# Kernel optimization log

Measured on AMD Instinct MI355X. Metric: run time of the kernel, lower is better.

## Reference

```python
import jax, jax.numpy as jnp
import numpy as np


def setup_inputs() -> dict:
    key = jax.random.key(0)
    kA, kB = jax.random.split(key)
    B, H, W, C = 1, 80, 80, 256  # NHWC backbone features; B must be 1 for the TF broadcast in the divide to be valid
    feature_A = jax.random.normal(kA, (B, H, W, C), dtype=jnp.float32)
    feature_B = jax.random.normal(kB, (B, H, W, C), dtype=jnp.float32)
    return {"feature_A": feature_A, "feature_B": feature_B}


def reference(feature_A, feature_B):
    # corr[b,i,j,k,l] = mean_c A[b,i,j,c] * B[b,k,l,c]
    # Expressed as a batched matmul instead of materializing the (H,W,H,W,C) intermediate.
    C = feature_A.shape[-1]
    corr = jnp.einsum('bijc,bklc->bijkl', feature_A, feature_B) / C  # [B,H,W,H,W]
    # penalty[b,i,j] = sqrt(sum_{k,l} corr^2)
    penalty = jnp.sqrt(jnp.sum(corr * corr, axis=(-1, -2)))  # [B,H,W]
    # Faithful to tf.math.divide: trailing-dim broadcasting of [B,H,W] against [B,H,W,H,W]
    # (valid because B == 1; penalty aligns to the (j,k,l) trailing axes exactly as in TF).
    return corr / penalty
```

## Files before the change

kernel.cpp:

```cpp
#include <hip/hip_runtime.h>

typedef __attribute__((ext_vector_type(8))) short bf16x8;
typedef __attribute__((ext_vector_type(4))) float f32x4;

#define M_TOT 6400
#define C_TOT 256
#define BM 128
#define BN 128
#define BK 32
#define NTILE 50
#define GK_CHUNKS 20
#define GK_STEPS  10

#define VMCNT0 asm volatile("s_waitcnt vmcnt(0)" ::: "memory")
#define VMCNT4 asm volatile("s_waitcnt vmcnt(4)" ::: "memory")
#define SBAR   __builtin_amdgcn_s_barrier()

__device__ __forceinline__ short f2bf(float f) {
    unsigned u = __float_as_uint(f);
    u = (u + 0x7fffu + ((u >> 16) & 1u)) >> 16;
    return (short)u;
}
__device__ __forceinline__ float bf2f(short s) {
    return __uint_as_float(((unsigned)(unsigned short)s) << 16);
}

__device__ __forceinline__ void gload16(const short* g, short* l) {
    __builtin_amdgcn_global_load_lds(
        (const __attribute__((address_space(1))) void*)g,
        (__attribute__((address_space(3))) void*)l, 16, 0, 0);
}


__global__ __launch_bounds__(256) void convert_a(const float* __restrict__ A,
                                                 short* __restrict__ Ab)
{
    const int n8 = M_TOT * C_TOT / 8;
    for (int i = blockIdx.x * blockDim.x + threadIdx.x; i < n8;
         i += gridDim.x * blockDim.x) {
        const float4 v0 = reinterpret_cast<const float4*>(A + (size_t)i * 8)[0];
        const float4 v1 = reinterpret_cast<const float4*>(A + (size_t)i * 8)[1];
        bf16x8 w;
        w[0]=f2bf(v0.x); w[1]=f2bf(v0.y); w[2]=f2bf(v0.z); w[3]=f2bf(v0.w);
        w[4]=f2bf(v1.x); w[5]=f2bf(v1.y); w[6]=f2bf(v1.z); w[7]=f2bf(v1.w);
        *reinterpret_cast<bf16x8*>(Ab + (size_t)i * 8) = w;
    }
}

__global__ __launch_bounds__(256) void convert_ab(const float* __restrict__ A,
                                                  const float* __restrict__ Bm,
                                                  short* __restrict__ Ab,
                                                  short* __restrict__ Bb)
{
    const int n8 = M_TOT * C_TOT / 8;
    for (int i = blockIdx.x * blockDim.x + threadIdx.x; i < 2 * n8;
         i += gridDim.x * blockDim.x) {
        const float* s = (i < n8) ? (A + (size_t)i * 8) : (Bm + (size_t)(i - n8) * 8);
        short* d       = (i < n8) ? (Ab + (size_t)i * 8) : (Bb + (size_t)(i - n8) * 8);
        const float4 v0 = reinterpret_cast<const float4*>(s)[0];
        const float4 v1 = reinterpret_cast<const float4*>(s)[1];
        bf16x8 w;
        w[0]=f2bf(v0.x); w[1]=f2bf(v0.y); w[2]=f2bf(v0.z); w[3]=f2bf(v0.w);
        w[4]=f2bf(v1.x); w[5]=f2bf(v1.y); w[6]=f2bf(v1.z); w[7]=f2bf(v1.w);
        *reinterpret_cast<bf16x8*>(d) = w;
    }
}

__global__ __launch_bounds__(256) void trans_b(const float* __restrict__ Bm,
                                               short* __restrict__ Bb,
                                               short* __restrict__ Bt)
{
    __shared__ __align__(16) short Lb[64][72];
    const int t  = threadIdx.x;
    const int n0 = blockIdx.x * 64;
    const int c0 = blockIdx.y * 64;
    const int r  = t >> 2;
    const int cb = (t & 3) * 16;

    const float4* src = reinterpret_cast<const float4*>(
        Bm + (size_t)(n0 + r) * C_TOT + c0 + cb);
    const float4 v0 = src[0], v1 = src[1], v2 = src[2], v3 = src[3];
    bf16x8 w0, w1;
    w0[0]=f2bf(v0.x); w0[1]=f2bf(v0.y); w0[2]=f2bf(v0.z); w0[3]=f2bf(v0.w);
    w0[4]=f2bf(v1.x); w0[5]=f2bf(v1.y); w0[6]=f2bf(v1.z); w0[7]=f2bf(v1.w);
    w1[0]=f2bf(v2.x); w1[1]=f2bf(v2.y); w1[2]=f2bf(v2.z); w1[3]=f2bf(v2.w);
    w1[4]=f2bf(v3.x); w1[5]=f2bf(v3.y); w1[6]=f2bf(v3.z); w1[7]=f2bf(v3.w);
    *reinterpret_cast<bf16x8*>(&Lb[r][cb])     = w0;
    *reinterpret_cast<bf16x8*>(&Lb[r][cb + 8]) = w1;
    short* brow = Bb + (size_t)(n0 + r) * C_TOT + c0 + cb;
    *reinterpret_cast<bf16x8*>(brow)     = w0;
    *reinterpret_cast<bf16x8*>(brow + 8) = w1;
    __syncthreads();

    #pragma unroll
    for (int p = 0; p < 2; ++p) {
        const int q = t + p * 256;
        const int c = q >> 3;
        const int h = q & 7;
        bf16x8 w;
        #pragma unroll
        for (int j = 0; j < 8; ++j) w[j] = Lb[h * 8 + j][c];
        *reinterpret_cast<bf16x8*>(&Bt[(size_t)(c0 + c) * M_TOT + n0 + h * 8]) = w;
    }
}


__device__ __forceinline__ void stage_tiles_g(const short* __restrict__ A,
                                              const short* __restrict__ B,
                                              int m0, int n0, int k0,
                                              int lda, int ldb,
                                              short* As, short* Bs,
                                              int wave, int lane)
{
    #pragma unroll
    for (int t = 0; t < 2; ++t) {
        const int c  = (wave * 2 + t) * 64 + lane;
        const int r  = c >> 2;
        const int g  = c & 3;
        const int sg = g ^ ((r >> 1) & 3);
        gload16(A + (size_t)(m0 + r) * lda + k0 + sg * 8, As + (wave * 2 + t) * 512);
        gload16(B + (size_t)(n0 + r) * ldb + k0 + sg * 8, Bs + (wave * 2 + t) * 512);
    }
}

template<int KSTEPS>
__device__ __forceinline__ void gemm_tile_g(const short* __restrict__ A,
                                            const short* __restrict__ B,
                                            int m0, int n0, int kbase,
                                            int lda, int ldb, int tid,
                                            short (*Sm)[2][4096],
                                            f32x4 acc[4][4])
{
    const int lane = tid & 63;
    const int wave = tid >> 6;
    const int rl   = lane & 15;
    const int g_rd = lane >> 4;
    const int wr   = wave >> 1;
    const int wc   = wave & 1;

    stage_tiles_g(A, B, m0, n0, kbase, lda, ldb, &Sm[0][0][0], &Sm[0][1][0], wave, lane);
    if (KSTEPS > 1)
        stage_tiles_g(A, B, m0, n0, kbase + BK, lda, ldb,
                      &Sm[1][0][0], &Sm[1][1][0], wave, lane);
    if (KSTEPS > 1) { VMCNT4; } else { VMCNT0; }
    SBAR;

    #pragma unroll
    for (int kt = 0; kt < KSTEPS; ++kt) {
        const int cur = kt % 3;
        if (kt + 2 < KSTEPS)
            stage_tiles_g(A, B, m0, n0, kbase + (kt + 2) * BK, lda, ldb,
                          &Sm[(kt + 2) % 3][0][0], &Sm[(kt + 2) % 3][1][0], wave, lane);

        bf16x8 af[4], bfr[4];
        #pragma unroll
        for (int mi = 0; mi < 4; ++mi) {
            const int r  = wr * 64 + mi * 16 + rl;
            const int sg = g_rd ^ ((r >> 1) & 3);
            af[mi] = *reinterpret_cast<const bf16x8*>(&Sm[cur][0][r * BK + sg * 8]);
        }
        #pragma unroll
        for (int ni = 0; ni < 4; ++ni) {
            const int r  = wc * 64 + ni * 16 + rl;
            const int sg = g_rd ^ ((r >> 1) & 3);
            bfr[ni] = *reinterpret_cast<const bf16x8*>(&Sm[cur][1][r * BK + sg * 8]);
        }
        #pragma unroll
        for (int mi = 0; mi < 4; ++mi)
            #pragma unroll
            for (int ni = 0; ni < 4; ++ni)
                acc[mi][ni] = __builtin_amdgcn_mfma_f32_16x16x32_bf16(
                    af[mi], bfr[ni], acc[mi][ni], 0, 0, 0);

        if (kt + 1 < KSTEPS) {
            if (kt + 2 < KSTEPS) { VMCNT4; } else { VMCNT0; }
            SBAR;
        }
    }
}


__global__ __launch_bounds__(256) void gemm_G(const short* __restrict__ Bt,
                                              float* __restrict__ Gp)
{
    __shared__ __align__(16) short Sm[3][2][4096];
    const int tid = threadIdx.x;
    const int m0 = blockIdx.y * BM, n0 = blockIdx.x * BN;
    const int z  = blockIdx.z;
    f32x4 acc[4][4] = {};
    gemm_tile_g<GK_STEPS>(Bt, Bt, m0, n0, z * (M_TOT / GK_CHUNKS),
                          M_TOT, M_TOT, tid, Sm, acc);

    float* dst = Gp + (size_t)z * (C_TOT * C_TOT);
    const int lane = tid & 63, rl = lane & 15;
    const int wave = tid >> 6, wr = wave >> 1, wc = wave & 1;
    #pragma unroll
    for (int mi = 0; mi < 4; ++mi)
        #pragma unroll
        for (int i = 0; i < 4; ++i) {
            const int m = m0 + wr * 64 + mi * 16 + (lane >> 4) * 4 + i;
            #pragma unroll
            for (int ni = 0; ni < 4; ++ni)
                dst[m * C_TOT + n0 + wc * 64 + ni * 16 + rl] = acc[mi][ni][i];
        }
}

__global__ __launch_bounds__(256) void g_reduce(const float* __restrict__ Gp,
                                                short* __restrict__ Gb)
{
    const int i4 = blockIdx.x * 256 + threadIdx.x;
    float4 s = make_float4(0.f, 0.f, 0.f, 0.f);
    for (int z = 0; z < GK_CHUNKS; ++z) {
        const float4 v = reinterpret_cast<const float4*>(
            Gp + (size_t)z * (C_TOT * C_TOT))[i4];
        s.x += v.x; s.y += v.y; s.z += v.z; s.w += v.w;
    }
    short4 o;
    o.x = f2bf(s.x); o.y = f2bf(s.y); o.z = f2bf(s.z); o.w = f2bf(s.w);
    reinterpret_cast<short4*>(Gb)[i4] = o;
}

__global__ __launch_bounds__(256) void penalty_G(const short* __restrict__ Ab,
                                                 const short* __restrict__ Gb,
                                                 float* __restrict__ P)
{
    __shared__ __align__(16) short Sm[3][2][4096];
    __shared__ float q_lds[BM];
    const int tid = threadIdx.x;
    const int m0 = blockIdx.x * BM;
    const int lane = tid & 63, rl = lane & 15;
    const int wave = tid >> 6, wr = wave >> 1, wc = wave & 1;

    if (tid < BM) q_lds[tid] = 0.0f;
    __syncthreads();

    #pragma unroll
    for (int nt = 0; nt < 2; ++nt) {
        f32x4 acc[4][4] = {};
        gemm_tile_g<8>(Ab, Gb, m0, nt * BN, 0, C_TOT, C_TOT, tid, Sm, acc);
        const int n0 = nt * BN;
        #pragma unroll
        for (int mi = 0; mi < 4; ++mi)
            #pragma unroll
            for (int i = 0; i < 4; ++i) {
                const int m = m0 + wr * 64 + mi * 16 + (lane >> 4) * 4 + i;
                float s = 0.0f;
                #pragma unroll
                for (int ni = 0; ni < 4; ++ni) {
                    const int cp = n0 + wc * 64 + ni * 16 + rl;
                    s += acc[mi][ni][i] * bf2f(Ab[(size_t)m * C_TOT + cp]);
                }
                s += __shfl_xor(s, 1);
                s += __shfl_xor(s, 2);
                s += __shfl_xor(s, 4);
                s += __shfl_xor(s, 8);
                if (rl == 0) atomicAdd(&q_lds[m - m0], s);
            }
        __syncthreads();
    }
    if (tid < BM) P[m0 + tid] = q_lds[tid];
}


__global__ __launch_bounds__(256) void gemm_out(const short* __restrict__ Ab,
                                                const short* __restrict__ Bb,
                                                const float* __restrict__ P,
                                                float* __restrict__ out)
{
    __shared__ __align__(16) short Sm[3][2][4096];
    const int tid = threadIdx.x;
    const int lane = tid & 63, rl = lane & 15;
    const int wave = tid >> 6, wr = wave >> 1, wc = wave & 1;

    const int nwg = NTILE * NTILE, q = nwg >> 3, r = nwg & 7;
    const int orig = blockIdx.x;
    const int xcd = orig & 7, idx = orig >> 3;
    const int wg = (xcd < r ? xcd * (q + 1) : r * (q + 1) + (xcd - r) * q) + idx;
    const int m0 = (wg / NTILE) * BM;
    const int n0 = (wg % NTILE) * BN;

    float rs[4];
    #pragma unroll
    for (int ni = 0; ni < 4; ++ni)
        rs[ni] = rsqrtf(P[n0 + wc * 64 + ni * 16 + rl]);

    f32x4 acc[4][4] = {};
    gemm_tile_g<8>(Ab, Bb, m0, n0, 0, C_TOT, C_TOT, tid, Sm, acc);

    SBAR;

    float* Es = reinterpret_cast<float*>(Sm) + wave * 1088;
    #pragma unroll
    for (int mi = 0; mi < 4; ++mi) {
        #pragma unroll
        for (int ni = 0; ni < 4; ++ni)
            #pragma unroll
            for (int i = 0; i < 4; ++i)
                Es[((lane >> 4) * 4 + i) * 68 + ni * 16 + rl] = acc[mi][ni][i] * rs[ni];
        #pragma unroll
        for (int it = 0; it < 4; ++it) {
            const int f   = it * 64 + lane;
            const int row = f >> 4;
            const int c4  = f & 15;
            const float4 v = *reinterpret_cast<const float4*>(&Es[row * 68 + c4 * 4]);
            const int m = m0 + wr * 64 + mi * 16 + row;
            *reinterpret_cast<float4*>(&out[(size_t)m * M_TOT + n0 + wc * 64 + c4 * 4]) = v;
        }
    }
}


__global__ __launch_bounds__(256) void gemm_penalty(const short* __restrict__ Ab,
                                                    const short* __restrict__ Bb,
                                                    float* __restrict__ P)
{
    __shared__ __align__(16) short Sm[3][2][4096];
    const int tid = threadIdx.x;
    const int m0 = blockIdx.y * BM, n0 = blockIdx.x * BN;
    f32x4 acc[4][4] = {};
    gemm_tile_g<8>(Ab, Bb, m0, n0, 0, C_TOT, C_TOT, tid, Sm, acc);

    const int lane = tid & 63, rl = lane & 15;
    const int wave = tid >> 6, wr = wave >> 1;
    #pragma unroll
    for (int mi = 0; mi < 4; ++mi) {
        #pragma unroll
        for (int i = 0; i < 4; ++i) {
            const int m = m0 + wr * 64 + mi * 16 + (lane >> 4) * 4 + i;
            float s = 0.0f;
            #pragma unroll
            for (int ni = 0; ni < 4; ++ni) {
                const float v = acc[mi][ni][i];
                s += v * v;
            }
            s += __shfl_xor(s, 1);
            s += __shfl_xor(s, 2);
            s += __shfl_xor(s, 4);
            s += __shfl_xor(s, 8);
            if (rl == 0) atomicAdd(&P[m], s);
        }
    }
}

__global__ __launch_bounds__(256) void gemm_out_plain(const short* __restrict__ Ab,
                                                      const short* __restrict__ Bb,
                                                      const float* __restrict__ P,
                                                      float* __restrict__ out)
{
    __shared__ __align__(16) short Sm[3][2][4096];
    const int tid = threadIdx.x;
    const int lane = tid & 63, rl = lane & 15;
    const int wave = tid >> 6, wr = wave >> 1, wc = wave & 1;
    const int m0 = blockIdx.y * BM, n0 = blockIdx.x * BN;

    float rs[4];
    #pragma unroll
    for (int ni = 0; ni < 4; ++ni)
        rs[ni] = rsqrtf(P[n0 + wc * 64 + ni * 16 + rl]);

    f32x4 acc[4][4] = {};
    gemm_tile_g<8>(Ab, Bb, m0, n0, 0, C_TOT, C_TOT, tid, Sm, acc);

    SBAR;

    float* Es = reinterpret_cast<float*>(Sm) + wave * 1088;
    #pragma unroll
    for (int mi = 0; mi < 4; ++mi) {
        #pragma unroll
        for (int ni = 0; ni < 4; ++ni)
            #pragma unroll
            for (int i = 0; i < 4; ++i)
                Es[((lane >> 4) * 4 + i) * 68 + ni * 16 + rl] = acc[mi][ni][i] * rs[ni];
        #pragma unroll
        for (int it = 0; it < 4; ++it) {
            const int f   = it * 64 + lane;
            const int row = f >> 4;
            const int c4  = f & 15;
            const float4 v = *reinterpret_cast<const float4*>(&Es[row * 68 + c4 * 4]);
            const int m = m0 + wr * 64 + mi * 16 + row;
            *reinterpret_cast<float4*>(&out[(size_t)m * M_TOT + n0 + wc * 64 + c4 * 4]) = v;
        }
    }
}


__global__ __launch_bounds__(256) void corr_gemm(const float* __restrict__ A,
                                                 const float* __restrict__ Bm,
                                                 float* __restrict__ out,
                                                 float* __restrict__ penalty)
{
    __shared__ short As[BM * BK];
    __shared__ short Bs[BN * BK];

    const int tid  = threadIdx.x;
    const int lane = tid & 63;
    const int wave = tid >> 6;
    const int wr   = wave >> 1;
    const int wc   = wave & 1;
    const int m0   = blockIdx.y * BM;
    const int n0   = blockIdx.x * BN;
    const int g_rd = lane >> 4;
    const int rl   = lane & 15;

    f32x4 acc[4][4] = {};

    for (int k0 = 0; k0 < C_TOT; k0 += BK) {
        #pragma unroll
        for (int half = 0; half < 2; ++half) {
            const int cc = tid + half * 256;
            const int r  = cc >> 2;
            const int g  = cc & 3;
            const int sg = g ^ ((r >> 1) & 3);

            const float4* pa = reinterpret_cast<const float4*>(
                A + (size_t)(m0 + r) * C_TOT + k0 + g * 8);
            float4 a0 = pa[0], a1 = pa[1];
            bf16x8 wa;
            wa[0]=f2bf(a0.x); wa[1]=f2bf(a0.y); wa[2]=f2bf(a0.z); wa[3]=f2bf(a0.w);
            wa[4]=f2bf(a1.x); wa[5]=f2bf(a1.y); wa[6]=f2bf(a1.z); wa[7]=f2bf(a1.w);
            *reinterpret_cast<bf16x8*>(&As[r * BK + sg * 8]) = wa;

            const float4* pb = reinterpret_cast<const float4*>(
                Bm + (size_t)(n0 + r) * C_TOT + k0 + g * 8);
            float4 b0 = pb[0], b1 = pb[1];
            bf16x8 wb;
            wb[0]=f2bf(b0.x); wb[1]=f2bf(b0.y); wb[2]=f2bf(b0.z); wb[3]=f2bf(b0.w);
            wb[4]=f2bf(b1.x); wb[5]=f2bf(b1.y); wb[6]=f2bf(b1.z); wb[7]=f2bf(b1.w);
            *reinterpret_cast<bf16x8*>(&Bs[r * BK + sg * 8]) = wb;
        }
        __syncthreads();

        bf16x8 af[4], bfr[4];
        #pragma unroll
        for (int mi = 0; mi < 4; ++mi) {
            const int r  = wr * 64 + mi * 16 + rl;
            const int sg = g_rd ^ ((r >> 1) & 3);
            af[mi] = *reinterpret_cast<const bf16x8*>(&As[r * BK + sg * 8]);
        }
        #pragma unroll
        for (int ni = 0; ni < 4; ++ni) {
            const int r  = wc * 64 + ni * 16 + rl;
            const int sg = g_rd ^ ((r >> 1) & 3);
            bfr[ni] = *reinterpret_cast<const bf16x8*>(&Bs[r * BK + sg * 8]);
        }
        #pragma unroll
        for (int mi = 0; mi < 4; ++mi)
            #pragma unroll
            for (int ni = 0; ni < 4; ++ni)
                acc[mi][ni] = __builtin_amdgcn_mfma_f32_16x16x32_bf16(
                    af[mi], bfr[ni], acc[mi][ni], 0, 0, 0);
        __syncthreads();
    }

    const float inv_c = 1.0f / (float)C_TOT;
    #pragma unroll
    for (int mi = 0; mi < 4; ++mi) {
        #pragma unroll
        for (int i = 0; i < 4; ++i) {
            const int m = m0 + wr * 64 + mi * 16 + (lane >> 4) * 4 + i;
            float s = 0.0f;
            #pragma unroll
            for (int ni = 0; ni < 4; ++ni) {
                const float v = acc[mi][ni][i] * inv_c;
                out[(size_t)m * M_TOT + n0 + wc * 64 + ni * 16 + rl] = v;
                s += v * v;
            }
            s += __shfl_xor(s, 1);
            s += __shfl_xor(s, 2);
            s += __shfl_xor(s, 4);
            s += __shfl_xor(s, 8);
            if (rl == 0) atomicAdd(&penalty[m], s);
        }
    }
}

__global__ __launch_bounds__(256) void scale_k(float* __restrict__ out,
                                               const float* __restrict__ penalty)
{
    const unsigned cols4 = M_TOT / 4;
    const unsigned total = (unsigned)M_TOT * cols4;
    float4* o4 = reinterpret_cast<float4*>(out);
    const float4* p4 = reinterpret_cast<const float4*>(penalty);
    for (unsigned idx = blockIdx.x * blockDim.x + threadIdx.x; idx < total;
         idx += gridDim.x * blockDim.x) {
        const unsigned n4 = idx % cols4;
        const float4 p = p4[n4];
        float4 v = o4[idx];
        v.x *= rsqrtf(p.x);
        v.y *= rsqrtf(p.y);
        v.z *= rsqrtf(p.z);
        v.w *= rsqrtf(p.w);
        o4[idx] = v;
    }
}


extern "C" void kernel_launch(void* const* d_in, const int* in_sizes, int n_in,
                              void* d_out, int out_size, void* d_ws, size_t ws_size,
                              hipStream_t stream) {
    const float* A = (const float*)d_in[0];
    const float* B = (const float*)d_in[1];
    float* out     = (float*)d_out;

    const size_t mat_sh = (size_t)M_TOT * C_TOT;
    const size_t sz_ab  = mat_sh * sizeof(short);
    const size_t sz_gb  = (size_t)C_TOT * C_TOT * sizeof(short);
    const size_t sz_p   = (size_t)M_TOT * sizeof(float);
    const size_t sz_gp  = (size_t)GK_CHUNKS * C_TOT * C_TOT * sizeof(float);
    const size_t need_full = 3 * sz_ab + sz_gb + sz_p + sz_gp;
    const size_t need_mid  = 2 * sz_ab + sz_p;

    dim3 grid2(NTILE, NTILE);

    if (ws_size >= need_full) {
        short* Ab = (short*)d_ws;
        short* Bb = Ab + mat_sh;
        short* Bt = Bb + mat_sh;
        short* Gb = Bt + mat_sh;
        float* P  = (float*)((char*)d_ws + 3 * sz_ab + sz_gb);
        float* Gp = (float*)((char*)d_ws + 3 * sz_ab + sz_gb + sz_p);

        convert_a<<<800, 256, 0, stream>>>(A, Ab);
        trans_b<<<dim3(M_TOT / 64, C_TOT / 64), 256, 0, stream>>>(B, Bb, Bt);
        gemm_G<<<dim3(2, 2, GK_CHUNKS), 256, 0, stream>>>(Bt, Gp);
        g_reduce<<<64, 256, 0, stream>>>(Gp, Gb);
        penalty_G<<<M_TOT / BM, 256, 0, stream>>>(Ab, Gb, P);
        gemm_out<<<NTILE * NTILE, 256, 0, stream>>>(Ab, Bb, P, out);
    } else if (ws_size >= need_mid) {
        short* Ab = (short*)d_ws;
        short* Bb = Ab + mat_sh;
        float* P  = (float*)(Bb + mat_sh);

        hipMemsetAsync(P, 0, sz_p, stream);
        convert_ab<<<1600, 256, 0, stream>>>(A, B, Ab, Bb);
        gemm_penalty<<<grid2, dim3(256), 0, stream>>>(Ab, Bb, P);
        gemm_out_plain<<<grid2, dim3(256), 0, stream>>>(Ab, Bb, P, out);
    } else {
        float* penalty = (float*)d_ws;
        hipMemsetAsync(penalty, 0, sz_p, stream);
        corr_gemm<<<grid2, dim3(256), 0, stream>>>(A, B, out, penalty);
        scale_k<<<2048, 256, 0, stream>>>(out, penalty);
    }
}
```

Baseline: 85.52 us.

## Fuse prep kernels, split penalty GEMM into quadrants, deepen Gram split-K

Merges the A conversion, B transpose and penalty zeroing into one prep launch, which removes a kernel launch and a memset. The Gram-matrix GEMM uses 40 K-chunks when workspace allows, giving more blocks in flight. The penalty kernel is split over a 4x grid of G quadrants that accumulate with global atomics, raising block count from 50 to 200. It also raises wave priority around the MFMA block and moves the penalty loads after the GEMM in the output kernel. The costs are more atomics, more partial-sum memory traffic in g_reduce, and a larger workspace requirement for the 40-chunk path.

```diff
diff --git a/kernel.cpp b/kernel.cpp
--- a/kernel.cpp
+++ b/kernel.cpp
@@ -9,8 +9,6 @@
 #define BN 128
 #define BK 32
 #define NTILE 50
-#define GK_CHUNKS 20
-#define GK_STEPS  10
 
 #define VMCNT0 asm volatile("s_waitcnt vmcnt(0)" ::: "memory")
 #define VMCNT4 asm volatile("s_waitcnt vmcnt(4)" ::: "memory")
@@ -32,18 +30,63 @@
 }
 
 
-__global__ __launch_bounds__(256) void convert_a(const float* __restrict__ A,
-                                                 short* __restrict__ Ab)
-{
-    const int n8 = M_TOT * C_TOT / 8;
-    for (int i = blockIdx.x * blockDim.x + threadIdx.x; i < n8;
-         i += gridDim.x * blockDim.x) {
-        const float4 v0 = reinterpret_cast<const float4*>(A + (size_t)i * 8)[0];
-        const float4 v1 = reinterpret_cast<const float4*>(A + (size_t)i * 8)[1];
-        bf16x8 w;
-        w[0]=f2bf(v0.x); w[1]=f2bf(v0.y); w[2]=f2bf(v0.z); w[3]=f2bf(v0.w);
-        w[4]=f2bf(v1.x); w[5]=f2bf(v1.y); w[6]=f2bf(v1.z); w[7]=f2bf(v1.w);
-        *reinterpret_cast<bf16x8*>(Ab + (size_t)i * 8) = w;
+__global__ __launch_bounds__(256) void prep(const float* __restrict__ A,
+                                            const float* __restrict__ Bm,
+                                            short* __restrict__ Ab,
+                                            short* __restrict__ Bb,
+                                            short* __restrict__ Bt,
+                                            float* __restrict__ P)
+{
+    __shared__ __align__(16) short Lb[64][72];
+    const int bid = blockIdx.x;
+    const int t   = threadIdx.x;
+
+    if (bid < 400) {
+        const int n0 = (bid % 100) * 64;
+        const int c0 = (bid / 100) * 64;
+        const int r  = t >> 2;
+        const int cb = (t & 3) * 16;
+
+        const float4* src = reinterpret_cast<const float4*>(
+            Bm + (size_t)(n0 + r) * C_TOT + c0 + cb);
+        const float4 v0 = src[0], v1 = src[1], v2 = src[2], v3 = src[3];
+        bf16x8 w0, w1;
+        w0[0]=f2bf(v0.x); w0[1]=f2bf(v0.y); w0[2]=f2bf(v0.z); w0[3]=f2bf(v0.w);
+        w0[4]=f2bf(v1.x); w0[5]=f2bf(v1.y); w0[6]=f2bf(v1.z); w0[7]=f2bf(v1.w);
+        w1[0]=f2bf(v2.x); w1[1]=f2bf(v2.y); w1[2]=f2bf(v2.z); w1[3]=f2bf(v2.w);
+        w1[4]=f2bf(v3.x); w1[5]=f2bf(v3.y); w1[6]=f2bf(v3.z); w1[7]=f2bf(v3.w);
+        *reinterpret_cast<bf16x8*>(&Lb[r][cb])     = w0;
+        *reinterpret_cast<bf16x8*>(&Lb[r][cb + 8]) = w1;
+        short* brow = Bb + (size_t)(n0 + r) * C_TOT + c0 + cb;
+        *reinterpret_cast<bf16x8*>(brow)     = w0;
+        *reinterpret_cast<bf16x8*>(brow + 8) = w1;
+        __syncthreads();
+
+        #pragma unroll
+        for (int p = 0; p < 2; ++p) {
+            const int q = t + p * 256;
+            const int c = q >> 3;
+            const int h = q & 7;
+            bf16x8 w;
+            #pragma unroll
+            for (int j = 0; j < 8; ++j) w[j] = Lb[h * 8 + j][c];
+            *reinterpret_cast<bf16x8*>(&Bt[(size_t)(c0 + c) * M_TOT + n0 + h * 8]) = w;
+        }
+    } else {
+        const int aid = bid - 400;
+        if (aid == 0)
+            for (int j = t; j < M_TOT; j += 256) P[j] = 0.0f;
+        const int base = aid * 2048;
+        #pragma unroll
+        for (int it = 0; it < 8; ++it) {
+            const int i = base + it * 256 + t;
+            const float4 v0 = reinterpret_cast<const float4*>(A + (size_t)i * 8)[0];
+            const float4 v1 = reinterpret_cast<const float4*>(A + (size_t)i * 8)[1];
+            bf16x8 w;
+            w[0]=f2bf(v0.x); w[1]=f2bf(v0.y); w[2]=f2bf(v0.z); w[3]=f2bf(v0.w);
+            w[4]=f2bf(v1.x); w[5]=f2bf(v1.y); w[6]=f2bf(v1.z); w[7]=f2bf(v1.w);
+            *reinterpret_cast<bf16x8*>(Ab + (size_t)i * 8) = w;
+        }
     }
 }
 
@@ -66,44 +109,6 @@
     }
 }
 
-__global__ __launch_bounds__(256) void trans_b(const float* __restrict__ Bm,
-                                               short* __restrict__ Bb,
-                                               short* __restrict__ Bt)
-{
-    __shared__ __align__(16) short Lb[64][72];
-    const int t  = threadIdx.x;
-    const int n0 = blockIdx.x * 64;
-    const int c0 = blockIdx.y * 64;
-    const int r  = t >> 2;
-    const int cb = (t & 3) * 16;
-
-    const float4* src = reinterpret_cast<const float4*>(
-        Bm + (size_t)(n0 + r) * C_TOT + c0 + cb);
-    const float4 v0 = src[0], v1 = src[1], v2 = src[2], v3 = src[3];
-    bf16x8 w0, w1;
-    w0[0]=f2bf(v0.x); w0[1]=f2bf(v0.y); w0[2]=f2bf(v0.z); w0[3]=f2bf(v0.w);
-    w0[4]=f2bf(v1.x); w0[5]=f2bf(v1.y); w0[6]=f2bf(v1.z); w0[7]=f2bf(v1.w);
-    w1[0]=f2bf(v2.x); w1[1]=f2bf(v2.y); w1[2]=f2bf(v2.z); w1[3]=f2bf(v2.w);
-    w1[4]=f2bf(v3.x); w1[5]=f2bf(v3.y); w1[6]=f2bf(v3.z); w1[7]=f2bf(v3.w);
-    *reinterpret_cast<bf16x8*>(&Lb[r][cb])     = w0;
-    *reinterpret_cast<bf16x8*>(&Lb[r][cb + 8]) = w1;
-    short* brow = Bb + (size_t)(n0 + r) * C_TOT + c0 + cb;
-    *reinterpret_cast<bf16x8*>(brow)     = w0;
-    *reinterpret_cast<bf16x8*>(brow + 8) = w1;
-    __syncthreads();
-
-    #pragma unroll
-    for (int p = 0; p < 2; ++p) {
-        const int q = t + p * 256;
-        const int c = q >> 3;
-        const int h = q & 7;
-        bf16x8 w;
-        #pragma unroll
-        for (int j = 0; j < 8; ++j) w[j] = Lb[h * 8 + j][c];
-        *reinterpret_cast<bf16x8*>(&Bt[(size_t)(c0 + c) * M_TOT + n0 + h * 8]) = w;
-    }
-}
-
 
 __device__ __forceinline__ void stage_tiles_g(const short* __restrict__ A,
                                               const short* __restrict__ B,
@@ -165,12 +170,14 @@
             const int sg = g_rd ^ ((r >> 1) & 3);
             bfr[ni] = *reinterpret_cast<const bf16x8*>(&Sm[cur][1][r * BK + sg * 8]);
         }
+        __builtin_amdgcn_s_setprio(1);
         #pragma unroll
         for (int mi = 0; mi < 4; ++mi)
             #pragma unroll
             for (int ni = 0; ni < 4; ++ni)
                 acc[mi][ni] = __builtin_amdgcn_mfma_f32_16x16x32_bf16(
                     af[mi], bfr[ni], acc[mi][ni], 0, 0, 0);
+        __builtin_amdgcn_s_setprio(0);
 
         if (kt + 1 < KSTEPS) {
             if (kt + 2 < KSTEPS) { VMCNT4; } else { VMCNT0; }
@@ -180,6 +187,7 @@
 }
 
 
+template<int STEPS>
 __global__ __launch_bounds__(256) void gemm_G(const short* __restrict__ Bt,
                                               float* __restrict__ Gp)
 {
@@ -188,8 +196,8 @@
     const int m0 = blockIdx.y * BM, n0 = blockIdx.x * BN;
     const int z  = blockIdx.z;
     f32x4 acc[4][4] = {};
-    gemm_tile_g<GK_STEPS>(Bt, Bt, m0, n0, z * (M_TOT / GK_CHUNKS),
-                          M_TOT, M_TOT, tid, Sm, acc);
+    gemm_tile_g<STEPS>(Bt, Bt, m0, n0, z * (STEPS * BK),
+                       M_TOT, M_TOT, tid, Sm, acc);
 
     float* dst = Gp + (size_t)z * (C_TOT * C_TOT);
     const int lane = tid & 63, rl = lane & 15;
@@ -206,11 +214,12 @@
 }
 
 __global__ __launch_bounds__(256) void g_reduce(const float* __restrict__ Gp,
-                                                short* __restrict__ Gb)
+                                                short* __restrict__ Gb,
+                                                int nchunks)
 {
     const int i4 = blockIdx.x * 256 + threadIdx.x;
     float4 s = make_float4(0.f, 0.f, 0.f, 0.f);
-    for (int z = 0; z < GK_CHUNKS; ++z) {
+    for (int z = 0; z < nchunks; ++z) {
         const float4 v = reinterpret_cast<const float4*>(
             Gp + (size_t)z * (C_TOT * C_TOT))[i4];
         s.x += v.x; s.y += v.y; s.z += v.z; s.w += v.w;
@@ -220,45 +229,38 @@
     reinterpret_cast<short4*>(Gb)[i4] = o;
 }
 
-__global__ __launch_bounds__(256) void penalty_G(const short* __restrict__ Ab,
+__global__ __launch_bounds__(256) void penalty_q(const short* __restrict__ Ab,
                                                  const short* __restrict__ Gb,
                                                  float* __restrict__ P)
 {
     __shared__ __align__(16) short Sm[3][2][4096];
-    __shared__ float q_lds[BM];
     const int tid = threadIdx.x;
     const int m0 = blockIdx.x * BM;
+    const int ci = blockIdx.y & 1, cj = blockIdx.y >> 1;
     const int lane = tid & 63, rl = lane & 15;
     const int wave = tid >> 6, wr = wave >> 1, wc = wave & 1;
 
-    if (tid < BM) q_lds[tid] = 0.0f;
-    __syncthreads();
-
-    #pragma unroll
-    for (int nt = 0; nt < 2; ++nt) {
-        f32x4 acc[4][4] = {};
-        gemm_tile_g<8>(Ab, Gb, m0, nt * BN, 0, C_TOT, C_TOT, tid, Sm, acc);
-        const int n0 = nt * BN;
-        #pragma unroll
-        for (int mi = 0; mi < 4; ++mi)
-            #pragma unroll
-            for (int i = 0; i < 4; ++i) {
-                const int m = m0 + wr * 64 + mi * 16 + (lane >> 4) * 4 + i;
-                float s = 0.0f;
-                #pragma unroll
-                for (int ni = 0; ni < 4; ++ni) {
-                    const int cp = n0 + wc * 64 + ni * 16 + rl;
-                    s += acc[mi][ni][i] * bf2f(Ab[(size_t)m * C_TOT + cp]);
-                }
-                s += __shfl_xor(s, 1);
-                s += __shfl_xor(s, 2);
-                s += __shfl_xor(s, 4);
-                s += __shfl_xor(s, 8);
-                if (rl == 0) atomicAdd(&q_lds[m - m0], s);
+    f32x4 acc[4][4] = {};
+    gemm_tile_g<4>(Ab, Gb + (size_t)(cj * BM) * C_TOT, m0, 0, ci * BM,
+                   C_TOT, C_TOT, tid, Sm, acc);
+
+    #pragma unroll
+    for (int mi = 0; mi < 4; ++mi)
+        #pragma unroll
+        for (int i = 0; i < 4; ++i) {
+            const int m = m0 + wr * 64 + mi * 16 + (lane >> 4) * 4 + i;
+            float s = 0.0f;
+            #pragma unroll
+            for (int ni = 0; ni < 4; ++ni) {
+                const int cp = cj * BM + wc * 64 + ni * 16 + rl;
+                s += acc[mi][ni][i] * bf2f(Ab[(size_t)m * C_TOT + cp]);
             }
-        __syncthreads();
-    }
-    if (tid < BM) P[m0 + tid] = q_lds[tid];
+            s += __shfl_xor(s, 1);
+            s += __shfl_xor(s, 2);
+            s += __shfl_xor(s, 4);
+            s += __shfl_xor(s, 8);
+            if (rl == 0) atomicAdd(&P[m], s);
+        }
 }
 
 
@@ -279,13 +281,13 @@
     const int m0 = (wg / NTILE) * BM;
     const int n0 = (wg % NTILE) * BN;
 
+    f32x4 acc[4][4] = {};
+    gemm_tile_g<8>(Ab, Bb, m0, n0, 0, C_TOT, C_TOT, tid, Sm, acc);
+
     float rs[4];
     #pragma unroll
     for (int ni = 0; ni < 4; ++ni)
         rs[ni] = rsqrtf(P[n0 + wc * 64 + ni * 16 + rl]);
-
-    f32x4 acc[4][4] = {};
-    gemm_tile_g<8>(Ab, Bb, m0, n0, 0, C_TOT, C_TOT, tid, Sm, acc);
 
     SBAR;
 
@@ -353,13 +355,13 @@
     const int wave = tid >> 6, wr = wave >> 1, wc = wave & 1;
     const int m0 = blockIdx.y * BM, n0 = blockIdx.x * BN;
 
+    f32x4 acc[4][4] = {};
+    gemm_tile_g<8>(Ab, Bb, m0, n0, 0, C_TOT, C_TOT, tid, Sm, acc);
+
     float rs[4];
     #pragma unroll
     for (int ni = 0; ni < 4; ++ni)
         rs[ni] = rsqrtf(P[n0 + wc * 64 + ni * 16 + rl]);
-
-    f32x4 acc[4][4] = {};
-    gemm_tile_g<8>(Ab, Bb, m0, n0, 0, C_TOT, C_TOT, tid, Sm, acc);
 
     SBAR;
 
@@ -506,13 +508,15 @@
     const size_t sz_ab  = mat_sh * sizeof(short);
     const size_t sz_gb  = (size_t)C_TOT * C_TOT * sizeof(short);
     const size_t sz_p   = (size_t)M_TOT * sizeof(float);
-    const size_t sz_gp  = (size_t)GK_CHUNKS * C_TOT * C_TOT * sizeof(float);
-    const size_t need_full = 3 * sz_ab + sz_gb + sz_p + sz_gp;
+    const size_t sz_gq  = (size_t)C_TOT * C_TOT * sizeof(float);
+    const size_t base_need = 3 * sz_ab + sz_gb + sz_p;
+    const size_t need_f40  = base_need + 40 * sz_gq;
+    const size_t need_f20  = base_need + 20 * sz_gq;
     const size_t need_mid  = 2 * sz_ab + sz_p;
 
     dim3 grid2(NTILE, NTILE);
 
-    if (ws_size >= need_full) {
+    if (ws_size >= need_f20) {
         short* Ab = (short*)d_ws;
         short* Bb = Ab + mat_sh;
         short* Bt = Bb + mat_sh;
@@ -520,11 +524,15 @@
         float* P  = (float*)((char*)d_ws + 3 * sz_ab + sz_gb);
         float* Gp = (float*)((char*)d_ws + 3 * sz_ab + sz_gb + sz_p);
 
-        convert_a<<<800, 256, 0, stream>>>(A, Ab);
-        trans_b<<<dim3(M_TOT / 64, C_TOT / 64), 256, 0, stream>>>(B, Bb, Bt);
-        gemm_G<<<dim3(2, 2, GK_CHUNKS), 256, 0, stream>>>(Bt, Gp);
-        g_reduce<<<64, 256, 0, stream>>>(Gp, Gb);
-        penalty_G<<<M_TOT / BM, 256, 0, stream>>>(Ab, Gb, P);
+        prep<<<500, 256, 0, stream>>>(A, B, Ab, Bb, Bt, P);
+        if (ws_size >= need_f40) {
+            gemm_G<5><<<dim3(2, 2, 40), 256, 0, stream>>>(Bt, Gp);
+            g_reduce<<<64, 256, 0, stream>>>(Gp, Gb, 40);
+        } else {
+            gemm_G<10><<<dim3(2, 2, 20), 256, 0, stream>>>(Bt, Gp);
+            g_reduce<<<64, 256, 0, stream>>>(Gp, Gb, 20);
+        }
+        penalty_q<<<dim3(NTILE, 4), 256, 0, stream>>>(Ab, Gb, P);
         gemm_out<<<NTILE * NTILE, 256, 0, stream>>>(Ab, Bb, P, out);
     } else if (ws_size >= need_mid) {
         short* Ab = (short*)d_ws;
```

Result: no change. 85.01 us (-0.6%).
